# Optimization experiments

Hardware: AMD Instinct MI355X
Metric: run time of the kernel (lower is better)

Reference implementation:

```python
import jax, jax.numpy as jnp
import numpy as np
from jax import lax

H = 64  # hidden_size == embedding_size


def gru_last_hidden(emb, W_ih, W_hh, b_ih, b_hh):
    """PyTorch single-layer GRU over seq [L, H]; returns final hidden [H].
    Gate order in stacked weights: r, z, n (PyTorch convention)."""
    def step(h, x):
        gi = W_ih @ x + b_ih            # [3H]
        gh = W_hh @ h + b_hh            # [3H]
        i_r, i_z, i_n = jnp.split(gi, 3)
        h_r, h_z, h_n = jnp.split(gh, 3)
        r = jax.nn.sigmoid(i_r + h_r)
        z = jax.nn.sigmoid(i_z + h_z)
        n = jnp.tanh(i_n + r * h_n)
        h_new = (1.0 - z) * n + z * h
        return h_new, None
    h0 = jnp.zeros((H,), dtype=emb.dtype)
    h_last, _ = lax.scan(step, h0, emb)
    return h_last


def setup_inputs() -> dict:
    key = jax.random.key(0)
    ks = jax.random.split(key, 12)
    N, D, A, V, L = 256, 128, 40, 128, 16
    F3_IN = N * (D + H + N)
    s = 0.02
    return {
        "obs": jax.random.normal(ks[0], (N, D), dtype=jnp.float32),
        "token_ids": jax.random.randint(ks[1], (L,), 0, V),
        "emb_table": jax.random.normal(ks[2], (V, H), dtype=jnp.float32) * s,
        "gru_Wih": jax.random.normal(ks[3], (3 * H, H), dtype=jnp.float32) * s,
        "gru_Whh": jax.random.normal(ks[4], (3 * H, H), dtype=jnp.float32) * s,
        "gru_bih": jnp.zeros((3 * H,), dtype=jnp.float32),
        "gru_bhh": jnp.zeros((3 * H,), dtype=jnp.float32),
        "f1_W": jax.random.normal(ks[5], (H, 2 * D), dtype=jnp.float32) * s,
        "f1_b": jnp.zeros((H,), dtype=jnp.float32),
        "f3_W1": jax.random.normal(ks[6], (512, F3_IN), dtype=jnp.float32) * s,
        "f3_b1": jnp.zeros((512,), dtype=jnp.float32),
        "f3_W2": jax.random.normal(ks[7], (A, 512), dtype=jnp.float32) * s,
        "f3_b2": jnp.zeros((A,), dtype=jnp.float32),
    }


def reference(obs, token_ids, emb_table, gru_Wih, gru_Whh, gru_bih, gru_bhh,
              f1_W, f1_b, f3_W1, f3_b1, f3_W2, f3_b2):
    N = obs.shape[0]
    # Encoder: embedding lookup + GRU, keep last timestep output
    emb = emb_table[token_ids]                       # [L, H]
    g_tilde = gru_last_hidden(emb, gru_Wih, gru_Whh, gru_bih, gru_bhh)  # [H]

    # Pairwise f1 + dot with g_tilde. f1(concat(o_i,o_j)) @ g = obs_i@Wa.T@g
    # + obs_j@Wb.T@g + b@g  (exact factorization of the linear over pairs).
    Wa, Wb = jnp.split(f1_W, 2, axis=1)              # each [H, D]
    u = obs @ (Wa.T @ g_tilde)                       # [N]  (outer index a)
    v = obs @ (Wb.T @ g_tilde)                       # [N]  (inner index b)
    Z = u[:, None] + v[None, :] + jnp.dot(f1_b, g_tilde)   # [N, N]

    # softmax over ALL N^2 entries (torch Softmax(dim=0) on the flat stack)
    p = jax.nn.softmax(Z.reshape(-1)).reshape(N, N)

    g_rep = jnp.broadcast_to(g_tilde, (N, H))
    x = jnp.concatenate([obs, g_rep, p], axis=1).reshape(-1)  # [N*(D+H+N)]

    h1 = jax.nn.relu(f3_W1 @ x + f3_b1)
    return f3_W2 @ h1 + f3_b2                         # [action_shape]
```

## Files before the change

kernel.cpp:

```cpp
#include <hip/hip_runtime.h>
#include <math.h>

#define H    64
#define N    256
#define D    128
#define L    16
#define SEG    448
#define SEG4   112
#define F3IN (N * SEG)
#define CHUNK_SEGS 64
#define CHUNK4 (CHUNK_SEGS * SEG4)

typedef float v4f __attribute__((ext_vector_type(4)));

__device__ __forceinline__ float sigmoidf_(float x) {
    return 1.0f / (1.0f + expf(-x));
}
__device__ __forceinline__ float dot4(float4 a, float4 b) {
    return a.x * b.x + a.y * b.y + a.z * b.z + a.w * b.w;
}

__global__ __launch_bounds__(256) void k_enc(
    const int* __restrict__ token_ids, const float* __restrict__ emb_table,
    const float* __restrict__ Wih, const float* __restrict__ Whh,
    const float* __restrict__ bih, const float* __restrict__ bhh,
    const float* __restrict__ f1W, const float* __restrict__ obs,
    float* __restrict__ g_out, float* __restrict__ eus_out,
    float* __restrict__ ev_out)
{
    __shared__ float emb[L][H];
    __shared__ float h[H];
    __shared__ float hnew[H];
    __shared__ float gi_s[3 * H];
    __shared__ float gh_s[3 * H];
    __shared__ float wa_s[D];
    __shared__ float wb_s[D];
    __shared__ float red[256];

    const int k = threadIdx.x;

    for (int idx = k; idx < L * H; idx += 256) {
        int t = idx >> 6, d = idx & 63;
        emb[t][d] = emb_table[token_ids[t] * H + d];
    }
    if (k < H) h[k] = 0.0f;

    float4 wih4[16], whh4[16];
    float bi = 0.0f, bh = 0.0f;
    if (k < 3 * H) {
        const float4* wi = (const float4*)(Wih + k * H);
        const float4* wh = (const float4*)(Whh + k * H);
#pragma unroll
        for (int c = 0; c < 16; ++c) { wih4[c] = wi[c]; whh4[c] = wh[c]; }
        bi = bih[k]; bh = bhh[k];
    }
    __syncthreads();

    for (int t = 0; t < L; ++t) {
        if (k < 3 * H) {
            const float4* et = (const float4*)emb[t];
            const float4* hv = (const float4*)h;
            float gi = bi, gh = bh;
#pragma unroll
            for (int c = 0; c < 16; ++c) {
                gi += dot4(wih4[c], et[c]);
                gh += dot4(whh4[c], hv[c]);
            }
            gi_s[k] = gi;
            gh_s[k] = gh;
        }
        __syncthreads();
        if (k < H) {
            float r = sigmoidf_(gi_s[k] + gh_s[k]);
            float z = sigmoidf_(gi_s[H + k] + gh_s[H + k]);
            float n = tanhf(gi_s[2 * H + k] + r * gh_s[2 * H + k]);
            hnew[k] = (1.0f - z) * n + z * h[k];
        }
        __syncthreads();
        if (k < H) h[k] = hnew[k];
        __syncthreads();
    }

    {
        float s = 0.0f;
#pragma unroll 8
        for (int kk = 0; kk < H; ++kk) s += f1W[kk * (2 * D) + k] * h[kk];
        if (k < D) wa_s[k] = s;
        else       wb_s[k - D] = s;
        if (k < H) g_out[k] = h[k];
    }
    __syncthreads();

    const float4* rowp = (const float4*)(obs + k * D);
    const float4* wav = (const float4*)wa_s;
    const float4* wbv = (const float4*)wb_s;
    float u = 0.0f, v = 0.0f;
#pragma unroll
    for (int c = 0; c < D / 4; ++c) {
        float4 o = rowp[c];
        u += dot4(o, wav[c]);
        v += dot4(o, wbv[c]);
    }

    red[k] = u; __syncthreads();
    for (int s = 128; s > 0; s >>= 1) { if (k < s) red[k] = fmaxf(red[k], red[k + s]); __syncthreads(); }
    const float mu = red[0]; __syncthreads();
    const float eui = expf(u - mu);
    red[k] = eui; __syncthreads();
    for (int s = 128; s > 0; s >>= 1) { if (k < s) red[k] += red[k + s]; __syncthreads(); }
    const float Su = red[0]; __syncthreads();

    red[k] = v; __syncthreads();
    for (int s = 128; s > 0; s >>= 1) { if (k < s) red[k] = fmaxf(red[k], red[k + s]); __syncthreads(); }
    const float mv = red[0]; __syncthreads();
    const float evi = expf(v - mv);
    red[k] = evi; __syncthreads();
    for (int s = 128; s > 0; s >>= 1) { if (k < s) red[k] += red[k + s]; __syncthreads(); }
    const float Sv = red[0];

    eus_out[k] = eui * (1.0f / (Su * Sv));
    ev_out[k]  = evi;
}

__global__ __launch_bounds__(256, 4) void k_mv(
    const float* __restrict__ W1, const float* __restrict__ obs,
    const float* __restrict__ g, const float* __restrict__ eus,
    const float* __restrict__ ev, float* __restrict__ partial)
{
    __shared__ float g_s[64];
    __shared__ float ev_s[256];
    __shared__ float eu_s[64];
    __shared__ float red[256];

    const int t = threadIdx.x;
    const int row = blockIdx.x >> 2, q = blockIdx.x & 3;

    if (t < 64) { g_s[t] = g[t]; eu_s[t] = eus[q * 64 + t]; }
    ev_s[t] = ev[t];
    __syncthreads();

    const v4f* wb = (const v4f*)W1 + (size_t)row * (F3IN / 4) + (size_t)q * CHUNK4;
    const float4* obs4 = (const float4*)obs + q * CHUNK_SEGS * (D / 4);

    float a0 = 0.0f, a1 = 0.0f, a2 = 0.0f, a3 = 0.0f;
#pragma unroll 7
    for (int k = 0; k < 28; ++k) {
        const int idx = t + k * 256;
        const int seg = idx / SEG4;
        const int c4  = idx - seg * SEG4;
        v4f w = __builtin_nontemporal_load(wb + idx);
        float4 o;
        if (c4 < 32) {
            o = obs4[seg * 32 + c4];
        } else if (c4 < 48) {
            o = ((const float4*)g_s)[c4 - 32];
        } else {
            float4 e = ((const float4*)ev_s)[c4 - 48];
            float m = eu_s[seg];
            o = make_float4(e.x * m, e.y * m, e.z * m, e.w * m);
        }
        float d = w[0] * o.x + w[1] * o.y + w[2] * o.z + w[3] * o.w;
        switch (k & 3) {
            case 0: a0 += d; break;
            case 1: a1 += d; break;
            case 2: a2 += d; break;
            default: a3 += d; break;
        }
    }
    float sum = (a0 + a1) + (a2 + a3);

    red[t] = sum; __syncthreads();
    for (int s = 128; s > 0; s >>= 1) {
        if (t < s) red[t] += red[t + s];
        __syncthreads();
    }
    if (t == 0) partial[blockIdx.x] = red[0];
}

__global__ __launch_bounds__(512) void k_finish(
    const float* __restrict__ partial, const float* __restrict__ b1,
    const float* __restrict__ W2, const float* __restrict__ b2,
    float* __restrict__ out)
{
    __shared__ float h1s[512];
    const int r = threadIdx.x;
    {
        float4 p = ((const float4*)partial)[r];
        h1s[r] = fmaxf(p.x + p.y + p.z + p.w + b1[r], 0.0f);
    }
    __syncthreads();

    const int wave = r >> 6, lane = r & 63;
    for (int row = wave; row < 40; row += 8) {
        float s = 0.0f;
#pragma unroll
        for (int c = 0; c < 8; ++c)
            s += W2[row * 512 + lane + c * 64] * h1s[lane + c * 64];
#pragma unroll
        for (int off = 32; off > 0; off >>= 1) s += __shfl_down(s, off, 64);
        if (lane == 0) out[row] = s + b2[row];
    }
}

extern "C" void kernel_launch(void* const* d_in, const int* in_sizes, int n_in,
                              void* d_out, int out_size, void* d_ws, size_t ws_size,
                              hipStream_t stream)
{
    const float* obs       = (const float*)d_in[0];
    const int*   token_ids = (const int*)  d_in[1];
    const float* emb_table = (const float*)d_in[2];
    const float* Wih       = (const float*)d_in[3];
    const float* Whh       = (const float*)d_in[4];
    const float* bih       = (const float*)d_in[5];
    const float* bhh       = (const float*)d_in[6];
    const float* f1W       = (const float*)d_in[7];
    const float* W1        = (const float*)d_in[9];
    const float* b1        = (const float*)d_in[10];
    const float* W2        = (const float*)d_in[11];
    const float* b2        = (const float*)d_in[12];

    float* ws   = (float*)d_ws;
    float* g    = ws;
    float* eus  = ws + 64;
    float* ev   = ws + 320;
    float* part = ws + 576;
    float* out  = (float*)d_out;

    k_enc<<<1, 256, 0, stream>>>(token_ids, emb_table, Wih, Whh, bih, bhh,
                                 f1W, obs, g, eus, ev);
    k_mv<<<2048, 256, 0, stream>>>(W1, obs, g, eus, ev, part);
    k_finish<<<1, 512, 0, stream>>>(part, b1, W2, b2, out);
}
```

Before: 71.86 us.

## Tile W1 GEMV by row groups, fuse finish via last-block counter, hoist GRU input projections

The big matvec now has each block handle 8 rows by one column slice of 16 segments. The activation slice is built once in registers and reused across those rows instead of being rebuilt per row. The separate finish kernel is removed: the last block to arrive, detected with an atomic counter reset in k_enc, reduces the partials and applies W2. The encoder precomputes all GRU input projections before the recurrence, drops one barrier per step, holds f1W and the obs rows in registers, and merges the two softmax reductions. The price is higher register pressure and a serial tail on one block.

```diff
diff --git a/kernel.cpp b/kernel.cpp
--- a/kernel.cpp
+++ b/kernel.cpp
@@ -5,11 +5,11 @@
 #define N    256
 #define D    128
 #define L    16
-#define SEG    448
 #define SEG4   112
-#define F3IN (N * SEG)
-#define CHUNK_SEGS 64
-#define CHUNK4 (CHUNK_SEGS * SEG4)
+#define F3IN (N * 448)
+#define ROWS_PB 8
+#define CGS   16
+#define NBLK  ((512 / ROWS_PB) * CGS)
 
 typedef float v4f __attribute__((ext_vector_type(4)));
 
@@ -20,178 +20,214 @@
     return a.x * b.x + a.y * b.y + a.z * b.z + a.w * b.w;
 }
 
-__global__ __launch_bounds__(256) void k_enc(
+__global__ __launch_bounds__(256, 1) void k_enc(
     const int* __restrict__ token_ids, const float* __restrict__ emb_table,
     const float* __restrict__ Wih, const float* __restrict__ Whh,
     const float* __restrict__ bih, const float* __restrict__ bhh,
     const float* __restrict__ f1W, const float* __restrict__ obs,
     float* __restrict__ g_out, float* __restrict__ eus_out,
-    float* __restrict__ ev_out)
+    float* __restrict__ ev_out, unsigned int* __restrict__ counter)
 {
-    __shared__ float emb[L][H];
-    __shared__ float h[H];
-    __shared__ float hnew[H];
-    __shared__ float gi_s[3 * H];
-    __shared__ float gh_s[3 * H];
+    __shared__ float emb_s[L * H];
+    __shared__ float gi_all[L * 192];
+    __shared__ float h_s[H];
+    __shared__ float gh_s[192];
     __shared__ float wa_s[D];
     __shared__ float wb_s[D];
     __shared__ float red[256];
+    __shared__ float red2[256];
 
     const int k = threadIdx.x;
-
-    for (int idx = k; idx < L * H; idx += 256) {
-        int t = idx >> 6, d = idx & 63;
-        emb[t][d] = emb_table[token_ids[t] * H + d];
-    }
-    if (k < H) h[k] = 0.0f;
+    if (k == 0) *counter = 0u;
+
+    {
+        int tok = token_ids[k >> 4];
+        ((float4*)emb_s)[k] = ((const float4*)emb_table)[tok * 16 + (k & 15)];
+    }
+    if (k < H) h_s[k] = 0.0f;
 
     float4 wih4[16], whh4[16];
     float bi = 0.0f, bh = 0.0f;
-    if (k < 3 * H) {
+    if (k < 192) {
         const float4* wi = (const float4*)(Wih + k * H);
         const float4* wh = (const float4*)(Whh + k * H);
 #pragma unroll
         for (int c = 0; c < 16; ++c) { wih4[c] = wi[c]; whh4[c] = wh[c]; }
         bi = bih[k]; bh = bhh[k];
     }
-    __syncthreads();
-
-    for (int t = 0; t < L; ++t) {
-        if (k < 3 * H) {
-            const float4* et = (const float4*)emb[t];
-            const float4* hv = (const float4*)h;
-            float gi = bi, gh = bh;
-#pragma unroll
-            for (int c = 0; c < 16; ++c) {
-                gi += dot4(wih4[c], et[c]);
-                gh += dot4(whh4[c], hv[c]);
+
+    float f1wreg[64];
+#pragma unroll
+    for (int kk = 0; kk < 64; ++kk) f1wreg[kk] = f1W[kk * 256 + k];
+
+    __syncthreads();
+
+    if (k < 192) {
+        float gi[L];
+#pragma unroll
+        for (int tt = 0; tt < L; ++tt) gi[tt] = bi;
+#pragma unroll
+        for (int c = 0; c < 16; ++c) {
+            float4 w = wih4[c];
+#pragma unroll
+            for (int tt = 0; tt < L; ++tt)
+                gi[tt] += dot4(w, ((const float4*)(emb_s + tt * 64))[c]);
+        }
+#pragma unroll
+        for (int tt = 0; tt < L; ++tt) gi_all[tt * 192 + k] = gi[tt];
+    }
+    __syncthreads();
+
+    for (int tt = 0; tt < L; ++tt) {
+        if (k < 192) {
+            const float4* hv = (const float4*)h_s;
+            float a0 = 0, a1 = 0, a2 = 0, a3 = 0;
+#pragma unroll
+            for (int c = 0; c < 16; c += 4) {
+                a0 += dot4(whh4[c],     hv[c]);
+                a1 += dot4(whh4[c + 1], hv[c + 1]);
+                a2 += dot4(whh4[c + 2], hv[c + 2]);
+                a3 += dot4(whh4[c + 3], hv[c + 3]);
             }
-            gi_s[k] = gi;
-            gh_s[k] = gh;
+            gh_s[k] = (a0 + a1) + (a2 + a3) + bh;
         }
         __syncthreads();
         if (k < H) {
-            float r = sigmoidf_(gi_s[k] + gh_s[k]);
-            float z = sigmoidf_(gi_s[H + k] + gh_s[H + k]);
-            float n = tanhf(gi_s[2 * H + k] + r * gh_s[2 * H + k]);
-            hnew[k] = (1.0f - z) * n + z * h[k];
-        }
-        __syncthreads();
-        if (k < H) h[k] = hnew[k];
+            float r = sigmoidf_(gi_all[tt * 192 + k] + gh_s[k]);
+            float z = sigmoidf_(gi_all[tt * 192 + 64 + k] + gh_s[64 + k]);
+            float n = tanhf(gi_all[tt * 192 + 128 + k] + r * gh_s[128 + k]);
+            h_s[k] = (1.0f - z) * n + z * h_s[k];
+        }
         __syncthreads();
     }
 
     {
         float s = 0.0f;
-#pragma unroll 8
-        for (int kk = 0; kk < H; ++kk) s += f1W[kk * (2 * D) + k] * h[kk];
+#pragma unroll
+        for (int kk = 0; kk < 64; ++kk) s += f1wreg[kk] * h_s[kk];
         if (k < D) wa_s[k] = s;
         else       wb_s[k - D] = s;
-        if (k < H) g_out[k] = h[k];
-    }
-    __syncthreads();
-
-    const float4* rowp = (const float4*)(obs + k * D);
-    const float4* wav = (const float4*)wa_s;
-    const float4* wbv = (const float4*)wb_s;
+        if (k < H) g_out[k] = h_s[k];
+    }
+    __syncthreads();
+
+    float4 orow[32];
+    {
+        const float4* rp = (const float4*)(obs + k * D);
+#pragma unroll
+        for (int c = 0; c < 32; ++c) orow[c] = rp[c];
+    }
     float u = 0.0f, v = 0.0f;
 #pragma unroll
-    for (int c = 0; c < D / 4; ++c) {
-        float4 o = rowp[c];
-        u += dot4(o, wav[c]);
-        v += dot4(o, wbv[c]);
-    }
-
-    red[k] = u; __syncthreads();
-    for (int s = 128; s > 0; s >>= 1) { if (k < s) red[k] = fmaxf(red[k], red[k + s]); __syncthreads(); }
-    const float mu = red[0]; __syncthreads();
-    const float eui = expf(u - mu);
-    red[k] = eui; __syncthreads();
-    for (int s = 128; s > 0; s >>= 1) { if (k < s) red[k] += red[k + s]; __syncthreads(); }
-    const float Su = red[0]; __syncthreads();
-
-    red[k] = v; __syncthreads();
-    for (int s = 128; s > 0; s >>= 1) { if (k < s) red[k] = fmaxf(red[k], red[k + s]); __syncthreads(); }
-    const float mv = red[0]; __syncthreads();
-    const float evi = expf(v - mv);
-    red[k] = evi; __syncthreads();
-    for (int s = 128; s > 0; s >>= 1) { if (k < s) red[k] += red[k + s]; __syncthreads(); }
-    const float Sv = red[0];
+    for (int c = 0; c < 32; ++c) {
+        u += dot4(orow[c], ((const float4*)wa_s)[c]);
+        v += dot4(orow[c], ((const float4*)wb_s)[c]);
+    }
+
+    red[k] = u; red2[k] = v; __syncthreads();
+    for (int s = 128; s > 0; s >>= 1) {
+        if (k < s) { red[k] = fmaxf(red[k], red[k + s]); red2[k] = fmaxf(red2[k], red2[k + s]); }
+        __syncthreads();
+    }
+    const float mu = red[0], mv = red2[0];
+    __syncthreads();
+    const float eui = expf(u - mu), evi = expf(v - mv);
+    red[k] = eui; red2[k] = evi; __syncthreads();
+    for (int s = 128; s > 0; s >>= 1) {
+        if (k < s) { red[k] += red[k + s]; red2[k] += red2[k + s]; }
+        __syncthreads();
+    }
+    const float Su = red[0], Sv = red2[0];
 
     eus_out[k] = eui * (1.0f / (Su * Sv));
     ev_out[k]  = evi;
 }
 
-__global__ __launch_bounds__(256, 4) void k_mv(
+__global__ __launch_bounds__(256) void k_mv(
     const float* __restrict__ W1, const float* __restrict__ obs,
     const float* __restrict__ g, const float* __restrict__ eus,
-    const float* __restrict__ ev, float* __restrict__ partial)
+    const float* __restrict__ ev, float* __restrict__ partial,
+    const float* __restrict__ b1, const float* __restrict__ W2,
+    const float* __restrict__ b2, float* __restrict__ out,
+    unsigned int* __restrict__ counter)
 {
-    __shared__ float g_s[64];
-    __shared__ float ev_s[256];
-    __shared__ float eu_s[64];
-    __shared__ float red[256];
-
-    const int t = threadIdx.x;
-    const int row = blockIdx.x >> 2, q = blockIdx.x & 3;
-
-    if (t < 64) { g_s[t] = g[t]; eu_s[t] = eus[q * 64 + t]; }
-    ev_s[t] = ev[t];
-    __syncthreads();
-
-    const v4f* wb = (const v4f*)W1 + (size_t)row * (F3IN / 4) + (size_t)q * CHUNK4;
-    const float4* obs4 = (const float4*)obs + q * CHUNK_SEGS * (D / 4);
-
-    float a0 = 0.0f, a1 = 0.0f, a2 = 0.0f, a3 = 0.0f;
-#pragma unroll 7
-    for (int k = 0; k < 28; ++k) {
-        const int idx = t + k * 256;
-        const int seg = idx / SEG4;
-        const int c4  = idx - seg * SEG4;
-        v4f w = __builtin_nontemporal_load(wb + idx);
-        float4 o;
-        if (c4 < 32) {
-            o = obs4[seg * 32 + c4];
-        } else if (c4 < 48) {
-            o = ((const float4*)g_s)[c4 - 32];
-        } else {
-            float4 e = ((const float4*)ev_s)[c4 - 48];
-            float m = eu_s[seg];
-            o = make_float4(e.x * m, e.y * m, e.z * m, e.w * m);
-        }
-        float d = w[0] * o.x + w[1] * o.y + w[2] * o.z + w[3] * o.w;
-        switch (k & 3) {
-            case 0: a0 += d; break;
-            case 1: a1 += d; break;
-            case 2: a2 += d; break;
-            default: a3 += d; break;
-        }
-    }
-    float sum = (a0 + a1) + (a2 + a3);
-
-    red[t] = sum; __syncthreads();
-    for (int s = 128; s > 0; s >>= 1) {
-        if (t < s) red[t] += red[t + s];
-        __syncthreads();
-    }
-    if (t == 0) partial[blockIdx.x] = red[0];
-}
-
-__global__ __launch_bounds__(512) void k_finish(
-    const float* __restrict__ partial, const float* __restrict__ b1,
-    const float* __restrict__ W2, const float* __restrict__ b2,
-    float* __restrict__ out)
-{
+    const int t  = threadIdx.x;
+    const int cg = blockIdx.x & 15;
+    const int rg = blockIdx.x >> 4;
+
+    v4f xr[7];
+    {
+        const float4* obs4 = (const float4*)obs;
+        const float4* g4   = (const float4*)g;
+        const float4* ev4  = (const float4*)ev;
+#pragma unroll
+        for (int j = 0; j < 7; ++j) {
+            int idx = t + j * 256;
+            int s   = idx / SEG4;
+            int c   = idx - s * SEG4;
+            int seg = cg * 16 + s;
+            float4 o;
+            if (c < 32)       o = obs4[seg * 32 + c];
+            else if (c < 48)  o = g4[c - 32];
+            else {
+                float4 e = ev4[c - 48];
+                float m = eus[seg];
+                o = make_float4(e.x * m, e.y * m, e.z * m, e.w * m);
+            }
+            xr[j] = (v4f){o.x, o.y, o.z, o.w};
+        }
+    }
+
+    const v4f* wbase = (const v4f*)W1 + (size_t)(rg * ROWS_PB) * (F3IN / 4)
+                     + (size_t)cg * 1792 + t;
+    float sums[ROWS_PB];
+#pragma unroll
+    for (int rr = 0; rr < ROWS_PB; ++rr) {
+        const v4f* w = wbase + (size_t)rr * (F3IN / 4);
+        float a0 = 0.0f, a1 = 0.0f;
+#pragma unroll
+        for (int j = 0; j < 7; ++j) {
+            v4f wv = __builtin_nontemporal_load(w + j * 256);
+            float d = wv[0] * xr[j][0] + wv[1] * xr[j][1]
+                    + wv[2] * xr[j][2] + wv[3] * xr[j][3];
+            if (j & 1) a1 += d; else a0 += d;
+        }
+        sums[rr] = a0 + a1;
+    }
+
+    __shared__ float red[ROWS_PB * 4];
+    __shared__ unsigned int last_s;
+    const int wave = t >> 6, lane = t & 63;
+#pragma unroll
+    for (int rr = 0; rr < ROWS_PB; ++rr) {
+        float s = sums[rr];
+#pragma unroll
+        for (int off = 32; off > 0; off >>= 1) s += __shfl_down(s, off, 64);
+        if (lane == 0) red[rr * 4 + wave] = s;
+    }
+    __syncthreads();
+    if (t < ROWS_PB) {
+        partial[blockIdx.x * 32 + t] =
+            red[t * 4] + red[t * 4 + 1] + red[t * 4 + 2] + red[t * 4 + 3];
+    }
+    __threadfence();
+    __syncthreads();
+    if (t == 0) last_s = (atomicAdd(counter, 1u) == (NBLK - 1)) ? 1u : 0u;
+    __syncthreads();
+    if (!last_s) return;
+    __threadfence();
+
     __shared__ float h1s[512];
-    const int r = threadIdx.x;
-    {
-        float4 p = ((const float4*)partial)[r];
-        h1s[r] = fmaxf(p.x + p.y + p.z + p.w + b1[r], 0.0f);
-    }
-    __syncthreads();
-
-    const int wave = r >> 6, lane = r & 63;
-    for (int row = wave; row < 40; row += 8) {
+    for (int r = t; r < 512; r += 256) {
+        const int rgb = r >> 3, rr = r & 7;
+        float s = 0.0f;
+#pragma unroll
+        for (int cgi = 0; cgi < CGS; ++cgi)
+            s += partial[(rgb * CGS + cgi) * 32 + rr];
+        h1s[r] = fmaxf(s + b1[r], 0.0f);
+    }
+    __syncthreads();
+    for (int row = wave; row < 40; row += 4) {
         float s = 0.0f;
 #pragma unroll
         for (int c = 0; c < 8; ++c)
@@ -219,15 +255,16 @@
     const float* W2        = (const float*)d_in[11];
     const float* b2        = (const float*)d_in[12];
 
-    float* ws   = (float*)d_ws;
-    float* g    = ws;
-    float* eus  = ws + 64;
-    float* ev   = ws + 320;
-    float* part = ws + 576;
-    float* out  = (float*)d_out;
+    float* ws      = (float*)d_ws;
+    float* g       = ws;
+    float* eus     = ws + 64;
+    float* ev      = ws + 320;
+    unsigned int* counter = (unsigned int*)(ws + 576);
+    float* partial = ws + 640;
+    float* out     = (float*)d_out;
 
     k_enc<<<1, 256, 0, stream>>>(token_ids, emb_table, Wih, Whh, bih, bhh,
-                                 f1W, obs, g, eus, ev);
-    k_mv<<<2048, 256, 0, stream>>>(W1, obs, g, eus, ev, part);
-    k_finish<<<1, 512, 0, stream>>>(part, b1, W2, b2, out);
-}
+                                 f1W, obs, g, eus, ev, counter);
+    k_mv<<<NBLK, 256, 0, stream>>>(W1, obs, g, eus, ev, partial,
+                                   b1, W2, b2, out, counter);
+}
```

Result: slower. 227.8 us (+217.0%).
